# Kernel optimization log

Measured on AMD Instinct MI355X. Metric: run time of the kernel, lower is better.

The kernel has to match this reference:

```python
import jax, jax.numpy as jnp
import numpy as np

NUM_EMBEDDING = 512
EMBEDDING_DIM = 64
COMMITMENT_COST = 0.25


def setup_inputs() -> dict:
    key = jax.random.key(0)
    k1, k2 = jax.random.split(key)
    inputs = jax.random.normal(k1, (32, EMBEDDING_DIM, 64, 64), dtype=jnp.float32)
    # nn.Embedding weight init: uniform(-1/K, 1/K)
    weight = jax.random.uniform(
        k2, (NUM_EMBEDDING, EMBEDDING_DIM), dtype=jnp.float32,
        minval=-1.0 / NUM_EMBEDDING, maxval=1.0 / NUM_EMBEDDING)
    return {"inputs": inputs, "weight": weight}


def reference(inputs, weight):
    B, C, H, W = inputs.shape  # C == EMBEDDING_DIM
    K = weight.shape[0]
    sg = jax.lax.stop_gradient

    # NCHW -> NHWC -> [N, D]
    x = jnp.transpose(inputs, (0, 2, 3, 1)).reshape(-1, C)

    distances = (jnp.sum(x * x, axis=1, keepdims=True)
                 + jnp.sum(weight * weight, axis=1)
                 - 2.0 * jnp.matmul(x, weight.T))
    encoding_indices = jnp.argmin(distances, axis=1)  # [N]

    # one-hot scatter, as in the original
    encodings = jax.nn.one_hot(encoding_indices, K, dtype=x.dtype)  # [N, K]
    # quantized = encodings @ E  (== gather E[idx])
    quantized = jnp.matmul(encodings, weight)  # [N, D]

    q_latent_loss = jnp.mean((sg(quantized) - x) ** 2)
    e_latent_loss = jnp.mean((quantized - sg(x)) ** 2)
    loss = q_latent_loss + COMMITMENT_COST * e_latent_loss

    # straight-through estimator
    quantized_st = x + sg(quantized - x)

    avg_probs = jnp.mean(encodings, axis=0)  # [K]
    perplexity = jnp.exp(-jnp.sum(avg_probs * jnp.log(avg_probs + 1e-10)))

    # [N, D] -> [B, H, W, D] -> [B, D, H, W]
    quantized_out = jnp.transpose(quantized_st.reshape(B, H, W, C), (0, 3, 1, 2))
    return loss, quantized_out, perplexity, encodings
```

## Files before the change

### kernel.cpp

```cpp
#include <hip/hip_runtime.h>

#define BHW 262144
#define OUT_Q_OFF 1
#define OUT_P_OFF 8388609
#define OUT_E_OFF 8388610


typedef __attribute__((ext_vector_type(8))) short short8;
typedef __attribute__((ext_vector_type(4))) float f32x4;
typedef __attribute__((ext_vector_type(2))) float f32x2;

__device__ __forceinline__ unsigned short f2bf(float f) {
    union { float f; unsigned u; } c; c.f = f;
    unsigned r = (c.u + 0x7FFFu + ((c.u >> 16) & 1u)) >> 16;
    return (unsigned short)r;
}

__global__ __launch_bounds__(512) void vq_init(const float* __restrict__ W, float* __restrict__ ws) {
    const int tid = blockIdx.x * 512 + threadIdx.x;
    if (tid < 512) {
        const float4* W4 = (const float4*)W;
        float s = 0.f;
#pragma unroll
        for (int i = 0; i < 16; ++i) {
            float4 v = W4[tid * 16 + i];
            s = fmaf(v.x, v.x, s); s = fmaf(v.y, v.y, s);
            s = fmaf(v.z, v.z, s); s = fmaf(v.w, v.w, s);
        }
        ws[768 + tid] = s;
    } else {
        const int c  = tid - 512;
        const int l  = c & 63;
        const int j  = (c >> 6) & 1;
        const int tn = c >> 7;
        const int n  = tn * 16 + (l & 15);
        const int k0 = j * 32 + ((l >> 4) & 3) * 8;
        const float* src = W + n * 64 + k0;
        unsigned h0 = f2bf(-2.f * src[0]) | ((unsigned)f2bf(-2.f * src[1]) << 16);
        unsigned h1 = f2bf(-2.f * src[2]) | ((unsigned)f2bf(-2.f * src[3]) << 16);
        unsigned h2 = f2bf(-2.f * src[4]) | ((unsigned)f2bf(-2.f * src[5]) << 16);
        unsigned h3 = f2bf(-2.f * src[6]) | ((unsigned)f2bf(-2.f * src[7]) << 16);
        uint4* dst = (uint4*)(ws + 1280);
        dst[c] = make_uint4(h0, h1, h2, h3);
    }
}

__global__ __launch_bounds__(64) void vq_main(const float* __restrict__ X,
                                              const float* __restrict__ W,
                                              float* __restrict__ out,
                                              float* __restrict__ ws) {
    const int l    = threadIdx.x;
    const int nlow = l & 15;
    const int kg   = l >> 4;
    const int rowbase = blockIdx.x * 16;
    const int b  = rowbase >> 12;
    const int h  = (rowbase >> 6) & 63;
    const int w0 = rowbase & 63;

    const float* xr = X + (size_t)b * BHW + (size_t)h * 64 + (w0 + nlow);
    float xf[16];
#pragma unroll
    for (int e = 0; e < 8; ++e) xf[e]     = xr[(size_t)(kg * 8 + e) * 4096];
#pragma unroll
    for (int e = 0; e < 8; ++e) xf[8 + e] = xr[(size_t)(32 + kg * 8 + e) * 4096];
    short8 a0, a1;
#pragma unroll
    for (int e = 0; e < 8; ++e) { a0[e] = (short)f2bf(xf[e]); a1[e] = (short)f2bf(xf[8 + e]); }

    const short8* __restrict__ B8  = (const short8*)(ws + 1280);
    const float*  __restrict__ wsq = ws + 768;
    float bS[4]; int bK[4];
#pragma unroll
    for (int r = 0; r < 4; ++r) { bS[r] = 3.4e38f; bK[r] = 0; }

#pragma unroll 2
    for (int tn = 0; tn < 32; ++tn) {
        short8 f0 = B8[tn * 128 + l];
        short8 f1 = B8[tn * 128 + 64 + l];
        const float wq = wsq[tn * 16 + nlow];
        f32x4 acc = {wq, wq, wq, wq};
        acc = __builtin_amdgcn_mfma_f32_16x16x32_bf16(a0, f0, acc, 0, 0, 0);
        acc = __builtin_amdgcn_mfma_f32_16x16x32_bf16(a1, f1, acc, 0, 0, 0);
        const int n = tn * 16 + nlow;
#pragma unroll
        for (int r = 0; r < 4; ++r) {
            if (acc[r] < bS[r]) { bS[r] = acc[r]; bK[r] = n; }
        }
    }
#pragma unroll
    for (int r = 0; r < 4; ++r) {
#pragma unroll
        for (int mask = 1; mask <= 8; mask <<= 1) {
            float os = __shfl_xor(bS[r], mask);
            int   ok = __shfl_xor(bK[r], mask);
            if (os < bS[r] || (os == bS[r] && ok < bK[r])) { bS[r] = os; bK[r] = ok; }
        }
    }

    int rowBk = 0;
    int myBk  = 0;
    f32x2* encB = (f32x2*)(out + OUT_E_OFF);
    const size_t Rbase = (size_t)rowbase;
#pragma unroll
    for (int m = 0; m < 16; ++m) {
        int bkm = __shfl(bK[m & 3], (m >> 2) * 16);
        if (nlow == m) rowBk = bkm;
        if (l == m)    myBk = bkm;
        f32x2* erow = encB + (Rbase + m) * 256;
#pragma unroll
        for (int c = 0; c < 4; ++c) {
            int p = c * 64 + l;
            f32x2 v;
            v.x = (bkm == 2 * p)     ? 1.f : 0.f;
            v.y = (bkm == 2 * p + 1) ? 1.f : 0.f;
            erow[p] = v;
        }
    }
    if (l < 16) atomicAdd((unsigned*)ws + 256 + myBk, 1u);

    const float4* W4 = (const float4*)W;
    float4 q0 = W4[rowBk * 16 + kg * 2];
    float4 q1 = W4[rowBk * 16 + kg * 2 + 1];
    float4 q2 = W4[rowBk * 16 + 8 + kg * 2];
    float4 q3 = W4[rowBk * 16 + 8 + kg * 2 + 1];
    float qv[16] = {q0.x, q0.y, q0.z, q0.w, q1.x, q1.y, q1.z, q1.w,
                    q2.x, q2.y, q2.z, q2.w, q3.x, q3.y, q3.z, q3.w};
    float lsum = 0.f;
    float* op = out + OUT_Q_OFF + (size_t)b * BHW + (size_t)h * 64 + (w0 + nlow);
#pragma unroll
    for (int e = 0; e < 8; ++e) {
        float d0 = qv[e] - xf[e];
        lsum = fmaf(d0, d0, lsum);
        op[(size_t)(kg * 8 + e) * 4096] = xf[e] + d0;
        float d1 = qv[8 + e] - xf[8 + e];
        lsum = fmaf(d1, d1, lsum);
        op[(size_t)(32 + kg * 8 + e) * 4096] = xf[8 + e] + d1;
    }

#pragma unroll
    for (int off = 32; off >= 1; off >>= 1) lsum += __shfl_down(lsum, off);
    if (l == 0) atomicAdd(ws + (blockIdx.x & 255), lsum);
}

__global__ __launch_bounds__(512) void vq_fin(const float* __restrict__ ws, float* __restrict__ out) {
    __shared__ float redP[8], redL[8];
    const int t = threadIdx.x;
    const unsigned* counts = (const unsigned*)ws + 256;
    float p = (float)counts[t] * (1.0f / 131072.0f);
    float s = p * logf(p + 1e-10f);
    float lp = (t < 256) ? ws[t] : 0.f;
#pragma unroll
    for (int off = 32; off >= 1; off >>= 1) {
        s  += __shfl_down(s, off);
        lp += __shfl_down(lp, off);
    }
    if ((t & 63) == 0) { redP[t >> 6] = s; redL[t >> 6] = lp; }
    __syncthreads();
    if (t == 0) {
        float tp = 0.f, tl = 0.f;
#pragma unroll
        for (int i = 0; i < 8; ++i) { tp += redP[i]; tl += redL[i]; }
        out[OUT_P_OFF] = expf(-tp);
        out[0] = tl * (1.25f / 8388608.0f);
    }
}

extern "C" void kernel_launch(void* const* d_in, const int* in_sizes, int n_in,
                              void* d_out, int out_size, void* d_ws, size_t ws_size,
                              hipStream_t stream) {
    const float* X = (const float*)d_in[0];
    const float* W = (const float*)d_in[1];
    float* out = (float*)d_out;
    float* ws  = (float*)d_ws;

    (void)hipMemsetAsync(d_ws, 0, 768 * sizeof(float), stream);
    vq_init<<<9, 512, 0, stream>>>(W, ws);
    vq_main<<<8192, 64, 0, stream>>>(X, W, out, ws);
    vq_fin<<<1, 512, 0, stream>>>(ws, out);
}
```

Baseline: 116.5 us.

## Move codebook histogram to final kernel and use nontemporal output stores

Global atomic increments of per-code counters in the main kernel are replaced by writing each row's chosen index to workspace. The final single-block kernel then builds the histogram in shared memory with LDS atomics. Output stores for the quantized tensor and the one-hot encodings become nontemporal, the encodings write is moved after the quantized write, and the distance loop unroll goes from 2 to 4. The trade-off is contended global atomics versus an extra 1 MB index write plus a serial 262K-element histogram pass in one block, which may lengthen the tail kernel.

```diff
diff --git a/kernel.cpp b/kernel.cpp
--- a/kernel.cpp
+++ b/kernel.cpp
@@ -5,6 +5,7 @@
 #define OUT_P_OFF 8388609
 #define OUT_E_OFF 8388610
 
+#define IDX_W 17664
 
 typedef __attribute__((ext_vector_type(8))) short short8;
 typedef __attribute__((ext_vector_type(4))) float f32x4;
@@ -73,7 +74,7 @@
 #pragma unroll
     for (int r = 0; r < 4; ++r) { bS[r] = 3.4e38f; bK[r] = 0; }
 
-#pragma unroll 2
+#pragma unroll 4
     for (int tn = 0; tn < 32; ++tn) {
         short8 f0 = B8[tn * 128 + l];
         short8 f1 = B8[tn * 128 + 64 + l];
@@ -97,32 +98,20 @@
         }
     }
 
-    int rowBk = 0;
-    int myBk  = 0;
-    f32x2* encB = (f32x2*)(out + OUT_E_OFF);
-    const size_t Rbase = (size_t)rowbase;
-#pragma unroll
-    for (int m = 0; m < 16; ++m) {
-        int bkm = __shfl(bK[m & 3], (m >> 2) * 16);
-        if (nlow == m) rowBk = bkm;
-        if (l == m)    myBk = bkm;
-        f32x2* erow = encB + (Rbase + m) * 256;
-#pragma unroll
-        for (int c = 0; c < 4; ++c) {
-            int p = c * 64 + l;
-            f32x2 v;
-            v.x = (bkm == 2 * p)     ? 1.f : 0.f;
-            v.y = (bkm == 2 * p + 1) ? 1.f : 0.f;
-            erow[p] = v;
-        }
-    }
-    if (l < 16) atomicAdd((unsigned*)ws + 256 + myBk, 1u);
+    const int src = (nlow >> 2) * 16;
+    const int sel = nlow & 3;
+    int g0 = __shfl(bK[0], src), g1 = __shfl(bK[1], src);
+    int g2 = __shfl(bK[2], src), g3 = __shfl(bK[3], src);
+    const int rowBk = sel == 0 ? g0 : sel == 1 ? g1 : sel == 2 ? g2 : g3;
 
     const float4* W4 = (const float4*)W;
     float4 q0 = W4[rowBk * 16 + kg * 2];
     float4 q1 = W4[rowBk * 16 + kg * 2 + 1];
     float4 q2 = W4[rowBk * 16 + 8 + kg * 2];
     float4 q3 = W4[rowBk * 16 + 8 + kg * 2 + 1];
+
+    if (l < 16) ((int*)ws)[IDX_W + rowbase + l] = rowBk;
+
     float qv[16] = {q0.x, q0.y, q0.z, q0.w, q1.x, q1.y, q1.z, q1.w,
                     q2.x, q2.y, q2.z, q2.w, q3.x, q3.y, q3.z, q3.w};
     float lsum = 0.f;
@@ -131,10 +120,26 @@
     for (int e = 0; e < 8; ++e) {
         float d0 = qv[e] - xf[e];
         lsum = fmaf(d0, d0, lsum);
-        op[(size_t)(kg * 8 + e) * 4096] = xf[e] + d0;
+        __builtin_nontemporal_store(xf[e] + d0, op + (size_t)(kg * 8 + e) * 4096);
         float d1 = qv[8 + e] - xf[8 + e];
         lsum = fmaf(d1, d1, lsum);
-        op[(size_t)(32 + kg * 8 + e) * 4096] = xf[8 + e] + d1;
+        __builtin_nontemporal_store(xf[8 + e] + d1, op + (size_t)(32 + kg * 8 + e) * 4096);
+    }
+
+    f32x2* encB = (f32x2*)(out + OUT_E_OFF);
+    const size_t Rbase = (size_t)rowbase;
+#pragma unroll
+    for (int m = 0; m < 16; ++m) {
+        const int bkm = __shfl(bK[m & 3], (m >> 2) * 16);
+        f32x2* erow = encB + (Rbase + m) * 256;
+#pragma unroll
+        for (int c = 0; c < 4; ++c) {
+            const int p = c * 64 + l;
+            f32x2 v;
+            v.x = (bkm == 2 * p)     ? 1.f : 0.f;
+            v.y = (bkm == 2 * p + 1) ? 1.f : 0.f;
+            __builtin_nontemporal_store(v, erow + p);
+        }
     }
 
 #pragma unroll
@@ -143,10 +148,22 @@
 }
 
 __global__ __launch_bounds__(512) void vq_fin(const float* __restrict__ ws, float* __restrict__ out) {
+    __shared__ unsigned hist[512];
     __shared__ float redP[8], redL[8];
     const int t = threadIdx.x;
-    const unsigned* counts = (const unsigned*)ws + 256;
-    float p = (float)counts[t] * (1.0f / 131072.0f);
+    hist[t] = 0u;
+    __syncthreads();
+    const uint4* __restrict__ idx4 = (const uint4*)((const int*)ws + IDX_W);
+#pragma unroll 4
+    for (int i = 0; i < 64; ++i) {
+        uint4 v = idx4[i * 512 + t];
+        atomicAdd(&hist[v.x], 1u);
+        atomicAdd(&hist[v.y], 1u);
+        atomicAdd(&hist[v.z], 1u);
+        atomicAdd(&hist[v.w], 1u);
+    }
+    __syncthreads();
+    float p = (float)hist[t] * (1.0f / 131072.0f);
     float s = p * logf(p + 1e-10f);
     float lp = (t < 256) ? ws[t] : 0.f;
 #pragma unroll
@@ -173,7 +190,7 @@
     float* out = (float*)d_out;
     float* ws  = (float*)d_ws;
 
-    (void)hipMemsetAsync(d_ws, 0, 768 * sizeof(float), stream);
+    (void)hipMemsetAsync(d_ws, 0, 256 * sizeof(float), stream);
     vq_init<<<9, 512, 0, stream>>>(W, ws);
     vq_main<<<8192, 64, 0, stream>>>(X, W, out, ws);
     vq_fin<<<1, 512, 0, stream>>>(ws, out);
```

After: 145.0 us. 24.4% more time.
